# Optimization experiments

Measured on AMD Instinct MI355X. Metric: run time of the kernel, lower is better.

Reference implementation:

```python
import jax, jax.numpy as jnp
import numpy as np


def setup_inputs() -> dict:
    key = jax.random.key(0)
    k1, k2, k3 = jax.random.split(key, 3)
    N, D, C, G = 200000, 256, 512, 512
    x = jax.random.normal(k1, (N, D), dtype=jnp.float32)
    centroid_weight = jax.random.normal(k2, (C, D), dtype=jnp.float32)
    graph = jnp.sort(jax.random.randint(k3, (N,), 0, G, dtype=jnp.int64))
    return {"x": x, "centroid_weight": centroid_weight, "graph": graph, "num_graphs": G}


def reference(x, centroid_weight, graph, num_graphs):
    # EuclideanManifold: exp map at origin is the identity; dist is the L2 norm.
    # Pairwise node-to-centroid L2 distances via the GEMM identity
    # ||a-b||^2 = ||a||^2 + ||b||^2 - 2 a.b  (same math as the expanded
    # unsqueeze/expand path, without materializing the [N, C, D] tensor).
    x_sq = jnp.sum(x * x, axis=-1, keepdims=True)              # [N, 1]
    c_sq = jnp.sum(centroid_weight * centroid_weight, axis=-1)  # [C]
    sq = x_sq + c_sq[None, :] - 2.0 * jnp.einsum("nd,cd->nc", x, centroid_weight)
    dist = jnp.sqrt(jnp.maximum(sq, 0.0))                       # [N, C]

    # AvgPooling: per-graph mean of node-to-centroid distances.
    sums = jax.ops.segment_sum(dist, graph, num_segments=num_graphs)           # [G, C]
    counts = jax.ops.segment_sum(jnp.ones((dist.shape[0],), dist.dtype), graph,
                                 num_segments=num_graphs)                      # [G]
    return sums / jnp.maximum(counts, 1.0)[:, None]
```

## Files before the change

kernel.cpp:

```cpp
#include <hip/hip_runtime.h>
#include <hip/hip_bf16.h>

typedef __attribute__((ext_vector_type(8))) short short8;
typedef __attribute__((ext_vector_type(4))) float f32x4;
typedef __attribute__((ext_vector_type(2))) unsigned int uint2v;
typedef __attribute__((ext_vector_type(4))) unsigned int uint4v;

#define DK 256
#define BM 128
#define BN 128
#define BK 64
#define NKT 4

__device__ __forceinline__ unsigned int pack2bf(float lo, float hi) {
  return __builtin_amdgcn_perm(__builtin_bit_cast(unsigned int, hi),
                               __builtin_bit_cast(unsigned int, lo), 0x07060302);
}

__global__ void __launch_bounds__(256)
prep_w(const float* __restrict__ w, unsigned short* __restrict__ wbf,
       float* __restrict__ csq) {
  const int b = blockIdx.x;
  const int ct = b >> 2, kt = b & 3;
  const int t = threadIdx.x;
  const int col = t >> 1, khalf = t & 1;
  const float* src = w + (size_t)(ct * BN + col) * DK + kt * BK + khalf * 32;
  unsigned char* dst = (unsigned char*)wbf + (size_t)b * 16384;
  const int sw = (col & 7) << 4;
  float s = 0.f;
  #pragma unroll
  for (int jc = 0; jc < 4; ++jc) {
    f32x4 v0 = *reinterpret_cast<const f32x4*>(src + jc * 8);
    f32x4 v1 = *reinterpret_cast<const f32x4*>(src + jc * 8 + 4);
    s += v0.x*v0.x + v0.y*v0.y + v0.z*v0.z + v0.w*v0.w
       + v1.x*v1.x + v1.y*v1.y + v1.z*v1.z + v1.w*v1.w;
    uint4v pk = { pack2bf(v0.x,v0.y), pack2bf(v0.z,v0.w),
                  pack2bf(v1.x,v1.y), pack2bf(v1.z,v1.w) };
    const int cidx = khalf * 4 + jc;
    *reinterpret_cast<uint4v*>(dst + ((col * 128 + cidx * 16) ^ sw)) = pk;
  }
  s += __shfl_xor(s, 1);
  if (khalf == 0) atomicAdd(&csq[ct * BN + col], s);
}

template<bool PREW>
__global__ void __launch_bounds__(256, 2)
centroid_gemm_pool(const float* __restrict__ x, const float* __restrict__ w,
                   const unsigned short* __restrict__ wbf,
                   const float* __restrict__ csqg, const int* __restrict__ graph,
                   float* __restrict__ outsum, int* __restrict__ cnt,
                   int N, int C, int row_tiles)
{
  __shared__ __align__(16) unsigned char lds_a[16384];
  __shared__ __align__(16) unsigned char lds_b[2][16384];
  __shared__ float xsq_lds[BM];
  __shared__ float csq_lds[BN];

  const int bid = blockIdx.x;
  const int xcd = bid & 7;
  const int j   = bid >> 3;
  const int ct  = j & 3;
  const int rt  = (j >> 2) * 8 + xcd;
  if (rt >= row_tiles) return;

  const int t    = threadIdx.x;
  const int lane = t & 63;
  const int wid  = t >> 6;
  const int wr   = wid >> 1, wc = wid & 1;
  const int h    = lane >> 4, l15 = lane & 15;

  const int g16 = t >> 4;
  const int sc4 = t & 15;
  const float* aptr[8];
  #pragma unroll
  for (int q = 0; q < 8; ++q) {
    int gr = rt * BM + q * 16 + g16;
    if (gr > N - 1) gr = N - 1;
    aptr[q] = x + (size_t)gr * DK + sc4 * 4;
  }
  const int awbase = (g16 * 128 + sc4 * 8) ^ ((g16 & 7) << 4);

  const int base_a = (wr * 8192 + l15 * 128 + h * 16) ^ ((l15 & 7) << 4);
  const int base_b = (wc * 8192 + l15 * 128 + h * 16) ^ ((l15 & 7) << 4);

  f32x4 acc[4][4];
  #pragma unroll
  for (int mt = 0; mt < 4; ++mt)
    #pragma unroll
    for (int nt = 0; nt < 4; ++nt)
      acc[mt][nt] = (f32x4){0.f, 0.f, 0.f, 0.f};
  f32x4 accx[4];
  #pragma unroll
  for (int mt = 0; mt < 4; ++mt) accx[mt] = (f32x4){0.f, 0.f, 0.f, 0.f};
  float cq[8] = {0.f,0.f,0.f,0.f,0.f,0.f,0.f,0.f};

  f32x4 ra[8];
  auto loadA = [&](int kt) {
    #pragma unroll
    for (int q = 0; q < 8; ++q)
      ra[q] = *reinterpret_cast<const f32x4*>(aptr[q] + kt * BK);
  };
  auto cvtA = [&]() {
    #pragma unroll
    for (int q = 0; q < 8; ++q) {
      f32x4 v = ra[q];
      uint2v pk = { pack2bf(v.x, v.y), pack2bf(v.z, v.w) };
      *reinterpret_cast<uint2v*>(lds_a + awbase + q * 2048) = pk;
    }
  };
  auto stageB = [&](int buf, int kt) {
    const unsigned short* src = wbf + (((size_t)ct * 4 + kt) << 13) + t * 8;
    unsigned char* dst = lds_b[buf] + t * 16;
    #pragma unroll
    for (int p = 0; p < 4; ++p)
      __builtin_amdgcn_global_load_lds(src + p * 2048, dst + p * 4096, 16, 0, 0);
  };
  auto stageBsync = [&](int buf, int kt) {
    #pragma unroll
    for (int q = 0; q < 8; ++q) {
      const int colq = q * 16 + g16;
      f32x4 v = *reinterpret_cast<const f32x4*>(
          w + (size_t)(ct * BN + colq) * DK + kt * BK + sc4 * 4);
      cq[q] += v.x*v.x + v.y*v.y + v.z*v.z + v.w*v.w;
      uint2v pk = { pack2bf(v.x, v.y), pack2bf(v.z, v.w) };
      *reinterpret_cast<uint2v*>(lds_b[buf] + awbase + q * 2048) = pk;
    }
  };
  auto compute = [&](unsigned char* lb) {
    #pragma unroll
    for (int kk = 0; kk < 2; ++kk) {
      short8 af[4], bfr[4];
      const int ka = base_a ^ (kk << 6);
      const int kb = base_b ^ (kk << 6);
      #pragma unroll
      for (int mt = 0; mt < 4; ++mt)
        af[mt] = *reinterpret_cast<const short8*>(lds_a + ka + mt * 2048);
      #pragma unroll
      for (int nt = 0; nt < 4; ++nt)
        bfr[nt] = *reinterpret_cast<const short8*>(lb + kb + nt * 2048);
      #pragma unroll
      for (int mt = 0; mt < 4; ++mt)
        #pragma unroll
        for (int nt = 0; nt < 4; ++nt)
          acc[mt][nt] = __builtin_amdgcn_mfma_f32_16x16x32_bf16(af[mt], bfr[nt], acc[mt][nt], 0, 0, 0);
      if (wc == 0) {
        #pragma unroll
        for (int mt = 0; mt < 4; ++mt)
          accx[mt] = __builtin_amdgcn_mfma_f32_16x16x32_bf16(af[mt], af[mt], accx[mt], 0, 0, 0);
      }
    }
  };

  loadA(0);
  if (PREW) stageB(0, 0); else stageBsync(0, 0);

  #pragma unroll
  for (int kt = 0; kt < NKT; ++kt) {
    const int cur = kt & 1;
    cvtA();
    if (kt + 1 < NKT) {
      loadA(kt + 1);
      if (PREW) stageB(cur ^ 1, kt + 1);
      else      stageBsync(cur ^ 1, kt + 1);
      asm volatile("s_waitcnt vmcnt(12)" ::: "memory");
    } else {
      asm volatile("s_waitcnt vmcnt(0)" ::: "memory");
    }
    asm volatile("s_waitcnt lgkmcnt(0)" ::: "memory");
    __builtin_amdgcn_sched_barrier(0);
    __builtin_amdgcn_s_barrier();
    __builtin_amdgcn_sched_barrier(0);
    compute(lds_b[cur]);
    __builtin_amdgcn_sched_barrier(0);
    __builtin_amdgcn_s_barrier();
    __builtin_amdgcn_sched_barrier(0);
  }

  if (wc == 0 && h == (l15 >> 2)) {
    #pragma unroll
    for (int mt = 0; mt < 4; ++mt)
      xsq_lds[wr * 64 + mt * 16 + l15] = accx[mt][l15 & 3];
  }
  if (!PREW) {
    #pragma unroll
    for (int q = 0; q < 8; ++q) {
      float sb = cq[q];
      sb += __shfl_xor(sb, 1); sb += __shfl_xor(sb, 2);
      sb += __shfl_xor(sb, 4); sb += __shfl_xor(sb, 8);
      if (l15 == 0) csq_lds[q * 16 + g16] = sb;
    }
  }
  __syncthreads();

  float xs[4][4], cs[4];
  #pragma unroll
  for (int mt = 0; mt < 4; ++mt)
    #pragma unroll
    for (int i = 0; i < 4; ++i)
      xs[mt][i] = xsq_lds[wr * 64 + mt * 16 + h * 4 + i];
  #pragma unroll
  for (int nt = 0; nt < 4; ++nt)
    cs[nt] = PREW ? csqg[ct * BN + wc * 64 + nt * 16 + l15]
                  : csq_lds[wc * 64 + nt * 16 + l15];
  #pragma unroll
  for (int mt = 0; mt < 4; ++mt)
    #pragma unroll
    for (int nt = 0; nt < 4; ++nt)
      #pragma unroll
      for (int i = 0; i < 4; ++i) {
        float dd = fmaf(-2.0f, acc[mt][nt][i], xs[mt][i] + cs[nt]);
        acc[mt][nt][i] = __builtin_amdgcn_sqrtf(fmaxf(dd, 0.f));
      }

  const int wbase = rt * BM + wr * 64;
  const int col0  = ct * BN + wc * 64;
  const int rowg  = wbase + lane;
  const int gl    = (rowg < N) ? graph[rowg] : -1;
  const int glp   = __shfl_up(gl, 1);
  const unsigned long long bmw = __ballot(lane == 0 || gl != glp);

  int s0 = 0;
  while (s0 < 64) {
    unsigned long long rest = (s0 < 63) ? (bmw >> (s0 + 1)) : 0ULL;
    const int e = rest ? s0 + 1 + __builtin_ctzll(rest) : 64;
    const int g = __shfl(gl, s0);
    if (g >= 0) {
      float p[4] = {0.f, 0.f, 0.f, 0.f};
      #pragma unroll
      for (int mt = 0; mt < 4; ++mt)
        #pragma unroll
        for (int i = 0; i < 4; ++i) {
          const int row = mt * 16 + h * 4 + i;
          const bool in = (row >= s0) && (row < e);
          #pragma unroll
          for (int nt = 0; nt < 4; ++nt)
            p[nt] += in ? acc[mt][nt][i] : 0.f;
        }
      #pragma unroll
      for (int nt = 0; nt < 4; ++nt) {
        p[nt] += __shfl_xor(p[nt], 16);
        p[nt] += __shfl_xor(p[nt], 32);
      }
      if (lane < 16) {
        #pragma unroll
        for (int nt = 0; nt < 4; ++nt)
          atomicAdd(&outsum[(size_t)g * C + col0 + nt * 16 + lane], p[nt]);
      }
      if (cnt && ct == 0 && wc == 0 && lane == 0)
        atomicAdd(&cnt[g], e - s0);
    }
    s0 = e;
  }
}

__global__ void __launch_bounds__(256)
divide_counts(float* __restrict__ out, const int* __restrict__ cnt, int C)
{
  const int g = blockIdx.x;
  const int c0 = cnt[g];
  const float inv = 1.0f / (float)(c0 > 1 ? c0 : 1);
  for (int c = threadIdx.x; c < C; c += 256)
    out[(size_t)g * C + c] *= inv;
}

__global__ void __launch_bounds__(128)
divide_by_count(float* __restrict__ out, const int* __restrict__ graph, int N, int C)
{
  const int g = blockIdx.x;
  int lo = 0, hi = N;
  while (lo < hi) { int mid = (lo + hi) >> 1; if (graph[mid] < g) lo = mid + 1; else hi = mid; }
  const int lb = lo;
  hi = N;
  while (lo < hi) { int mid = (lo + hi) >> 1; if (graph[mid] <= g) lo = mid + 1; else hi = mid; }
  const int cntg = lo - lb;
  const float inv = 1.0f / (float)(cntg > 1 ? cntg : 1);
  for (int c = threadIdx.x; c < C; c += blockDim.x)
    out[(size_t)g * C + c] *= inv;
}

extern "C" void kernel_launch(void* const* d_in, const int* in_sizes, int n_in,
                              void* d_out, int out_size, void* d_ws, size_t ws_size,
                              hipStream_t stream) {
  const float* x     = (const float*)d_in[0];
  const float* w     = (const float*)d_in[1];
  const int*   graph = (const int*)d_in[2];
  const int N = in_sizes[2];
  const int D = in_sizes[0] / N;
  const int C = in_sizes[1] / D;
  const int G = out_size / C;

  const int row_tiles = (N + BM - 1) / BM;
  const int rgroups   = (row_tiles + 7) / 8;
  const int grid      = rgroups * 8 * (C / BN);

  const size_t wbf_bytes = (size_t)16 * 16384;
  const size_t csq_off   = wbf_bytes;
  const size_t cnt_off   = wbf_bytes + (size_t)C * 4;
  const bool prew     = ws_size >= cnt_off + (size_t)G * 4;
  const bool have_cnt = prew || ws_size >= (size_t)G * 4;

  unsigned short* wbf = (unsigned short*)d_ws;
  float* csq = (float*)((char*)d_ws + csq_off);
  int*   cnt = prew ? (int*)((char*)d_ws + cnt_off)
                    : (have_cnt ? (int*)d_ws : nullptr);

  hipMemsetAsync(d_out, 0, (size_t)out_size * sizeof(float), stream);
  if (cnt) hipMemsetAsync(cnt, 0, (size_t)G * sizeof(int), stream);

  if (prew) {
    hipMemsetAsync(csq, 0, (size_t)C * sizeof(float), stream);
    prep_w<<<dim3(16), dim3(256), 0, stream>>>(w, wbf, csq);
    centroid_gemm_pool<true><<<dim3(grid), dim3(256), 0, stream>>>(
        x, w, wbf, csq, graph, (float*)d_out, cnt, N, C, row_tiles);
  } else {
    centroid_gemm_pool<false><<<dim3(grid), dim3(256), 0, stream>>>(
        x, w, wbf, csq, graph, (float*)d_out, cnt, N, C, row_tiles);
  }

  if (cnt)
    divide_counts<<<dim3(G), dim3(256), 0, stream>>>((float*)d_out, cnt, C);
  else
    divide_by_count<<<dim3(G), dim3(128), 0, stream>>>((float*)d_out, graph, N, C);
}
```

Baseline: 116.2 us.

## Process multiple row tiles per block with cross-tile prefetch

Each block now handles a chunk of up to four consecutive row tiles instead of one. At the end of each tile's K loop it prefetches the next tile's first A slice, its B slice and its graph labels, so loads overlap the epilogue. This amortizes block launch and prologue cost and removes the pipeline bubble at each tile start, at the cost of a quarter as many blocks. That gives less parallelism for hiding latency and more tail imbalance. B and the centroid norms are re-staged per tile, and the norms are computed only on the first tile.

Result: slower. 140.2 us (+20.6%).

```diff
diff --git a/kernel.cpp b/kernel.cpp
--- a/kernel.cpp
+++ b/kernel.cpp
@@ -11,6 +11,7 @@
 #define BN 128
 #define BK 64
 #define NKT 4
+#define RPB 4
 
 __device__ __forceinline__ unsigned int pack2bf(float lo, float hi) {
   return __builtin_amdgcn_perm(__builtin_bit_cast(unsigned int, hi),
@@ -60,8 +61,11 @@
   const int xcd = bid & 7;
   const int j   = bid >> 3;
   const int ct  = j & 3;
-  const int rt  = (j >> 2) * 8 + xcd;
-  if (rt >= row_tiles) return;
+  const int chunk = (j >> 2) * 8 + xcd;
+  const int n_chunks = (row_tiles + RPB - 1) / RPB;
+  if (chunk >= n_chunks) return;
+  const int chunk0 = chunk * RPB;
+  const int vt = min(RPB, row_tiles - chunk0);
 
   const int t    = threadIdx.x;
   const int lane = t & 63;
@@ -72,12 +76,14 @@
   const int g16 = t >> 4;
   const int sc4 = t & 15;
   const float* aptr[8];
-  #pragma unroll
-  for (int q = 0; q < 8; ++q) {
-    int gr = rt * BM + q * 16 + g16;
-    if (gr > N - 1) gr = N - 1;
-    aptr[q] = x + (size_t)gr * DK + sc4 * 4;
-  }
+  auto setA = [&](int rt) {
+    #pragma unroll
+    for (int q = 0; q < 8; ++q) {
+      int gr = rt * BM + q * 16 + g16;
+      if (gr > N - 1) gr = N - 1;
+      aptr[q] = x + (size_t)gr * DK + sc4 * 4;
+    }
+  };
   const int awbase = (g16 * 128 + sc4 * 8) ^ ((g16 & 7) << 4);
 
   const int base_a = (wr * 8192 + l15 * 128 + h * 16) ^ ((l15 & 7) << 4);
@@ -115,13 +121,13 @@
     for (int p = 0; p < 4; ++p)
       __builtin_amdgcn_global_load_lds(src + p * 2048, dst + p * 4096, 16, 0, 0);
   };
-  auto stageBsync = [&](int buf, int kt) {
+  auto stageBsync = [&](int buf, int kt, bool accum) {
     #pragma unroll
     for (int q = 0; q < 8; ++q) {
       const int colq = q * 16 + g16;
       f32x4 v = *reinterpret_cast<const f32x4*>(
           w + (size_t)(ct * BN + colq) * DK + kt * BK + sc4 * 4);
-      cq[q] += v.x*v.x + v.y*v.y + v.z*v.z + v.w*v.w;
+      if (accum) cq[q] += v.x*v.x + v.y*v.y + v.z*v.z + v.w*v.w;
       uint2v pk = { pack2bf(v.x, v.y), pack2bf(v.z, v.w) };
       *reinterpret_cast<uint2v*>(lds_b[buf] + awbase + q * 2048) = pk;
     }
@@ -151,105 +157,131 @@
     }
   };
 
+  auto loadG = [&](int rt) {
+    int rg = rt * BM + wr * 64 + lane;
+    return graph[rg < N ? rg : (N - 1)];
+  };
+
+  setA(chunk0);
   loadA(0);
-  if (PREW) stageB(0, 0); else stageBsync(0, 0);
-
-  #pragma unroll
-  for (int kt = 0; kt < NKT; ++kt) {
-    const int cur = kt & 1;
-    cvtA();
-    if (kt + 1 < NKT) {
-      loadA(kt + 1);
-      if (PREW) stageB(cur ^ 1, kt + 1);
-      else      stageBsync(cur ^ 1, kt + 1);
-      asm volatile("s_waitcnt vmcnt(12)" ::: "memory");
-    } else {
-      asm volatile("s_waitcnt vmcnt(0)" ::: "memory");
-    }
-    asm volatile("s_waitcnt lgkmcnt(0)" ::: "memory");
-    __builtin_amdgcn_sched_barrier(0);
-    __builtin_amdgcn_s_barrier();
-    __builtin_amdgcn_sched_barrier(0);
-    compute(lds_b[cur]);
-    __builtin_amdgcn_sched_barrier(0);
-    __builtin_amdgcn_s_barrier();
-    __builtin_amdgcn_sched_barrier(0);
-  }
-
-  if (wc == 0 && h == (l15 >> 2)) {
+  if (PREW) stageB(0, 0); else stageBsync(0, 0, true);
+  int gl_cur = loadG(chunk0);
+  int gl_nxt = 0;
+
+  for (int r2 = 0; r2 < RPB; ++r2) {
+    if (r2 >= vt) break;
+    const int rt = chunk0 + r2;
+    #pragma unroll
+    for (int kt = 0; kt < NKT; ++kt) {
+      const int cur = kt & 1;
+      cvtA();
+      const bool last = (r2 == vt - 1) && (kt == NKT - 1);
+      if (!last) {
+        if (kt == NKT - 1) {
+          setA(rt + 1);
+          gl_nxt = loadG(rt + 1);
+        }
+        loadA((kt + 1) & 3);
+        if (PREW) stageB(cur ^ 1, (kt + 1) & 3);
+        else      stageBsync(cur ^ 1, (kt + 1) & 3, r2 == 0 && kt == 0);
+        asm volatile("s_waitcnt vmcnt(12)" ::: "memory");
+      } else {
+        asm volatile("s_waitcnt vmcnt(0)" ::: "memory");
+      }
+      asm volatile("s_waitcnt lgkmcnt(0)" ::: "memory");
+      __builtin_amdgcn_sched_barrier(0);
+      __builtin_amdgcn_s_barrier();
+      __builtin_amdgcn_sched_barrier(0);
+      compute(lds_b[cur]);
+      __builtin_amdgcn_sched_barrier(0);
+      __builtin_amdgcn_s_barrier();
+      __builtin_amdgcn_sched_barrier(0);
+    }
+
+    if (wc == 0 && h == (l15 >> 2)) {
+      #pragma unroll
+      for (int mt = 0; mt < 4; ++mt)
+        xsq_lds[wr * 64 + mt * 16 + l15] = accx[mt][l15 & 3];
+    }
+    if (!PREW && r2 == 0) {
+      #pragma unroll
+      for (int q = 0; q < 8; ++q) {
+        float sb = cq[q];
+        sb += __shfl_xor(sb, 1); sb += __shfl_xor(sb, 2);
+        sb += __shfl_xor(sb, 4); sb += __shfl_xor(sb, 8);
+        if (l15 == 0) csq_lds[q * 16 + g16] = sb;
+      }
+    }
+    __syncthreads();
+
+    float xs[4][4], cs[4];
     #pragma unroll
     for (int mt = 0; mt < 4; ++mt)
-      xsq_lds[wr * 64 + mt * 16 + l15] = accx[mt][l15 & 3];
-  }
-  if (!PREW) {
-    #pragma unroll
-    for (int q = 0; q < 8; ++q) {
-      float sb = cq[q];
-      sb += __shfl_xor(sb, 1); sb += __shfl_xor(sb, 2);
-      sb += __shfl_xor(sb, 4); sb += __shfl_xor(sb, 8);
-      if (l15 == 0) csq_lds[q * 16 + g16] = sb;
-    }
-  }
-  __syncthreads();
-
-  float xs[4][4], cs[4];
-  #pragma unroll
-  for (int mt = 0; mt < 4; ++mt)
-    #pragma unroll
-    for (int i = 0; i < 4; ++i)
-      xs[mt][i] = xsq_lds[wr * 64 + mt * 16 + h * 4 + i];
-  #pragma unroll
-  for (int nt = 0; nt < 4; ++nt)
-    cs[nt] = PREW ? csqg[ct * BN + wc * 64 + nt * 16 + l15]
-                  : csq_lds[wc * 64 + nt * 16 + l15];
-  #pragma unroll
-  for (int mt = 0; mt < 4; ++mt)
+      #pragma unroll
+      for (int i = 0; i < 4; ++i)
+        xs[mt][i] = xsq_lds[wr * 64 + mt * 16 + h * 4 + i];
     #pragma unroll
     for (int nt = 0; nt < 4; ++nt)
-      #pragma unroll
-      for (int i = 0; i < 4; ++i) {
-        float dd = fmaf(-2.0f, acc[mt][nt][i], xs[mt][i] + cs[nt]);
-        acc[mt][nt][i] = __builtin_amdgcn_sqrtf(fmaxf(dd, 0.f));
-      }
-
-  const int wbase = rt * BM + wr * 64;
-  const int col0  = ct * BN + wc * 64;
-  const int rowg  = wbase + lane;
-  const int gl    = (rowg < N) ? graph[rowg] : -1;
-  const int glp   = __shfl_up(gl, 1);
-  const unsigned long long bmw = __ballot(lane == 0 || gl != glp);
-
-  int s0 = 0;
-  while (s0 < 64) {
-    unsigned long long rest = (s0 < 63) ? (bmw >> (s0 + 1)) : 0ULL;
-    const int e = rest ? s0 + 1 + __builtin_ctzll(rest) : 64;
-    const int g = __shfl(gl, s0);
-    if (g >= 0) {
-      float p[4] = {0.f, 0.f, 0.f, 0.f};
-      #pragma unroll
-      for (int mt = 0; mt < 4; ++mt)
+      cs[nt] = PREW ? csqg[ct * BN + wc * 64 + nt * 16 + l15]
+                    : csq_lds[wc * 64 + nt * 16 + l15];
+    #pragma unroll
+    for (int mt = 0; mt < 4; ++mt)
+      #pragma unroll
+      for (int nt = 0; nt < 4; ++nt)
         #pragma unroll
         for (int i = 0; i < 4; ++i) {
-          const int row = mt * 16 + h * 4 + i;
-          const bool in = (row >= s0) && (row < e);
+          float dd = fmaf(-2.0f, acc[mt][nt][i], xs[mt][i] + cs[nt]);
+          acc[mt][nt][i] = __builtin_amdgcn_sqrtf(fmaxf(dd, 0.f));
+        }
+
+    const int wbase = rt * BM + wr * 64;
+    const int col0  = ct * BN + wc * 64;
+    const int rowg  = wbase + lane;
+    const int gl    = (rowg < N) ? gl_cur : -1;
+    const int glp   = __shfl_up(gl, 1);
+    const unsigned long long bmw = __ballot(lane == 0 || gl != glp);
+
+    int s0 = 0;
+    while (s0 < 64) {
+      unsigned long long rest = (s0 < 63) ? (bmw >> (s0 + 1)) : 0ULL;
+      const int e = rest ? s0 + 1 + __builtin_ctzll(rest) : 64;
+      const int g = __shfl(gl, s0);
+      if (g >= 0) {
+        float p[4] = {0.f, 0.f, 0.f, 0.f};
+        #pragma unroll
+        for (int mt = 0; mt < 4; ++mt)
+          #pragma unroll
+          for (int i = 0; i < 4; ++i) {
+            const int row = mt * 16 + h * 4 + i;
+            const bool in = (row >= s0) && (row < e);
+            #pragma unroll
+            for (int nt = 0; nt < 4; ++nt)
+              p[nt] += in ? acc[mt][nt][i] : 0.f;
+          }
+        #pragma unroll
+        for (int nt = 0; nt < 4; ++nt) {
+          p[nt] += __shfl_xor(p[nt], 16);
+          p[nt] += __shfl_xor(p[nt], 32);
+        }
+        if (lane < 16) {
           #pragma unroll
           for (int nt = 0; nt < 4; ++nt)
-            p[nt] += in ? acc[mt][nt][i] : 0.f;
+            atomicAdd(&outsum[(size_t)g * C + col0 + nt * 16 + lane], p[nt]);
         }
-      #pragma unroll
-      for (int nt = 0; nt < 4; ++nt) {
-        p[nt] += __shfl_xor(p[nt], 16);
-        p[nt] += __shfl_xor(p[nt], 32);
+        if (cnt && ct == 0 && wc == 0 && lane == 0)
+          atomicAdd(&cnt[g], e - s0);
       }
-      if (lane < 16) {
-        #pragma unroll
-        for (int nt = 0; nt < 4; ++nt)
-          atomicAdd(&outsum[(size_t)g * C + col0 + nt * 16 + lane], p[nt]);
-      }
-      if (cnt && ct == 0 && wc == 0 && lane == 0)
-        atomicAdd(&cnt[g], e - s0);
-    }
-    s0 = e;
+      s0 = e;
+    }
+
+    #pragma unroll
+    for (int mt = 0; mt < 4; ++mt) {
+      #pragma unroll
+      for (int nt = 0; nt < 4; ++nt)
+        acc[mt][nt] = (f32x4){0.f, 0.f, 0.f, 0.f};
+      accx[mt] = (f32x4){0.f, 0.f, 0.f, 0.f};
+    }
+    gl_cur = gl_nxt;
   }
 }
 
@@ -290,8 +322,9 @@
   const int G = out_size / C;
 
   const int row_tiles = (N + BM - 1) / BM;
-  const int rgroups   = (row_tiles + 7) / 8;
-  const int grid      = rgroups * 8 * (C / BN);
+  const int n_chunks  = (row_tiles + RPB - 1) / RPB;
+  const int cgroups   = (n_chunks + 7) / 8;
+  const int grid      = cgroups * 8 * (C / BN);
 
   const size_t wbf_bytes = (size_t)16 * 16384;
   const size_t csq_off   = wbf_bytes;
```
